# Optimization experiments

Hardware: AMD Instinct MI355X
Metric: run time of the kernel (lower is better)

Reference implementation:

```python
import jax, jax.numpy as jnp
import numpy as np

QMIN, QMAX = -128.0, 127.0  # int8 range


def _fake_int_cast(t):
    # Emulates .to(torch.int8) on an already-clamped float tensor:
    # truncation toward zero, then back to float.
    return jnp.trunc(t)


def setup_inputs() -> dict:
    key = jax.random.key(0)
    k_x, k_w, k_ws, k_is, k_b = jax.random.split(key, 5)
    B, S, IN, OUT = 4, 2048, 4096, 4096
    x = jax.random.normal(k_x, (B, S, IN), dtype=jnp.float32)
    # quant_weight buffer holds int8 values (stored here as fp32 integers),
    # produced by quantizing a dense fp weight with per-out-channel scales.
    weight_scale = jax.random.uniform(k_ws, (OUT, 1), dtype=jnp.float32, minval=0.005, maxval=0.02)
    w_fp = jax.random.normal(k_w, (OUT, IN), dtype=jnp.float32) * 0.02
    quant_weight = jnp.trunc(jnp.clip(w_fp / weight_scale, QMIN, QMAX))
    input_scale = jax.random.uniform(k_is, (1,), dtype=jnp.float32, minval=0.01, maxval=0.03)
    bias = jax.random.normal(k_b, (OUT,), dtype=jnp.float32)
    return {"x": x, "quant_weight": quant_weight, "weight_scale": weight_scale,
            "input_scale": input_scale, "bias": bias}


def reference(x, quant_weight, weight_scale, input_scale, bias):
    # quantize input: clamp(x/scale) -> int8 (trunc toward zero) -> float
    quant_input = _fake_int_cast(jnp.clip(x / input_scale, QMIN, QMAX))
    # int8 matmul performed in fp32: [B,S,IN] @ [OUT,IN]^T -> [B,S,OUT]
    quant_output = jnp.einsum("bsi,oi->bso", quant_input, quant_weight)
    # dequantize with combined per-out-channel scale, viewed [1,1,OUT]
    scale = (weight_scale * input_scale).reshape((1,) * (quant_output.ndim - 1) + (-1,))
    output = quant_output * scale
    output = output + bias
    return output
```

## Files before the change

### kernel.cpp

```cpp
#include <hip/hip_runtime.h>


using v4i = __attribute__((ext_vector_type(4))) int;

typedef const __attribute__((address_space(1))) signed char gc_t;
typedef __attribute__((address_space(3))) signed char lc_t;

constexpr int BM = 256;
constexpr int BN = 256;
constexpr int BK = 128;
constexpr int TILE_BYTES = BM * BK;


__device__ __forceinline__ int quant4(const float4 f, float s) {
    int a = (int)fminf(fmaxf(f.x / s, -128.0f), 127.0f);
    int b = (int)fminf(fmaxf(f.y / s, -128.0f), 127.0f);
    int c = (int)fminf(fmaxf(f.z / s, -128.0f), 127.0f);
    int d = (int)fminf(fmaxf(f.w / s, -128.0f), 127.0f);
    return (a & 0xff) | ((b & 0xff) << 8) | ((c & 0xff) << 16) | ((d & 0xff) << 24);
}

__global__ void quant_x_kernel(const float4* __restrict__ x,
                               const float* __restrict__ scale,
                               int* __restrict__ out, int n4) {
    const float s = scale[0];
    int i = blockIdx.x * blockDim.x + threadIdx.x;
    if (i >= n4) return;
    out[i] = quant4(x[i], s);
}

__global__ void quant_w_kernel(const float4* __restrict__ w,
                               int* __restrict__ out, int n4) {
    int i = blockIdx.x * blockDim.x + threadIdx.x;
    if (i >= n4) return;
    float4 f = w[i];
    out[i] = ((int)f.x & 0xff) | (((int)f.y & 0xff) << 8) |
             (((int)f.z & 0xff) << 16) | (((int)f.w & 0xff) << 24);
}


#define STAGE_TILE(dstbuf, kbyte)                                              \
    do {                                                                       \
        const signed char* _pa = pA + (size_t)(kbyte);                         \
        const signed char* _pb = pB + (size_t)(kbyte);                         \
        lc_t* _la = (lc_t*)(smem + (dstbuf) * (2 * TILE_BYTES) +               \
                            (wid * 8) * BK);                                   \
        lc_t* _lb = (lc_t*)(smem + (dstbuf) * (2 * TILE_BYTES) + TILE_BYTES +  \
                            (wid * 8) * BK);                                   \
        _Pragma("unroll")                                                      \
        for (int c = 0; c < 4; ++c) {                                          \
            __builtin_amdgcn_global_load_lds(                                  \
                (gc_t*)(_pa + (size_t)(c * 64) * Kz), _la + c * 64 * BK,       \
                16, 0, 0);                                                     \
            __builtin_amdgcn_global_load_lds(                                  \
                (gc_t*)(_pb + (size_t)(c * 64) * Kz), _lb + c * 64 * BK,       \
                16, 0, 0);                                                     \
        }                                                                      \
    } while (0)

__global__ __launch_bounds__(512, 2) void gemm_i8_kernel(
    const signed char* __restrict__ Aq,
    const signed char* __restrict__ Wq,
    const float* __restrict__ wscale,
    const float* __restrict__ iscale,
    const float* __restrict__ bias,
    float* __restrict__ C,
    int M, int N, int K)
{
    __shared__ signed char smem[2 * 2 * TILE_BYTES];

    const int tid  = threadIdx.x;
    const int wid  = tid >> 6;
    const int lane = tid & 63;
    const int wm   = (wid >> 2) * 128;
    const int wn   = (wid & 3) * 64;

    const int nwg = gridDim.x;
    int wg = blockIdx.x;
    if ((nwg & 7) == 0) wg = (wg & 7) * (nwg >> 3) + (wg >> 3);
    const int ntx = N / BN;
    const int m0 = (wg / ntx) * BM;
    const int n0 = (wg % ntx) * BN;

    const int srow   = lane >> 3;
    const int gchunk = (lane & 7) ^ srow;

    const int fr = lane & 15;
    const int qh = lane >> 4;
    const int coff0 = ((0 * 4 + qh) ^ (fr & 7)) * 16;
    const int coff1 = ((1 * 4 + qh) ^ (fr & 7)) * 16;

    v4i acc[8][4];
#pragma unroll
    for (int i = 0; i < 8; ++i)
#pragma unroll
        for (int j = 0; j < 4; ++j) acc[i][j] = (v4i){0, 0, 0, 0};

    const size_t Kz = (size_t)K;
    const signed char* pA = Aq + (size_t)(m0 + wid * 8 + srow) * Kz + gchunk * 16;
    const signed char* pB = Wq + (size_t)(n0 + wid * 8 + srow) * Kz + gchunk * 16;

    const int NT = K / BK;

    STAGE_TILE(0, 0);
    STAGE_TILE(1, BK);

    for (int t = 0; t < NT; ++t) {
        const int cur = t & 1;
        if (t + 1 < NT) {
            asm volatile("s_waitcnt vmcnt(8)" ::: "memory");
        } else {
            asm volatile("s_waitcnt vmcnt(0)" ::: "memory");
        }
        __builtin_amdgcn_s_barrier();

        const signed char* Ab = smem + cur * (2 * TILE_BYTES);
        const signed char* Bb = Ab + TILE_BYTES;

        v4i bf[4][2];
        v4i af[2][2];

#pragma unroll
        for (int p = 0; p < 4; ++p) {
            if (p == 0) {
#pragma unroll
                for (int nt = 0; nt < 4; ++nt) {
                    const signed char* br = Bb + (size_t)(wn + nt * 16 + fr) * BK;
                    bf[nt][0] = *(const v4i*)(br + coff0);
                    bf[nt][1] = *(const v4i*)(br + coff1);
                }
            }
#pragma unroll
            for (int i = 0; i < 2; ++i) {
                const signed char* ar =
                    Ab + (size_t)(wm + (2 * p + i) * 16 + fr) * BK;
                af[i][0] = *(const v4i*)(ar + coff0);
                af[i][1] = *(const v4i*)(ar + coff1);
            }
            __builtin_amdgcn_s_barrier();
            __builtin_amdgcn_sched_barrier(0);
            __builtin_amdgcn_s_setprio(1);
#pragma unroll
            for (int s = 0; s < 2; ++s)
#pragma unroll
                for (int i = 0; i < 2; ++i)
#pragma unroll
                    for (int nt = 0; nt < 4; ++nt)
                        acc[2 * p + i][nt] = __builtin_amdgcn_mfma_i32_16x16x64_i8(
                            af[i][s], bf[nt][s], acc[2 * p + i][nt], 0, 0, 0);
            __builtin_amdgcn_s_setprio(0);
            __builtin_amdgcn_sched_barrier(0);
            __builtin_amdgcn_s_barrier();
        }

        if (t + 2 < NT) {
            asm volatile("" ::: "memory");
            STAGE_TILE(cur, (size_t)(t + 2) * BK);
            asm volatile("" ::: "memory");
        }
    }

    const float is = iscale[0];
#pragma unroll
    for (int nt = 0; nt < 4; ++nt) {
        const int col = n0 + wn + nt * 16 + fr;
        const float sc = wscale[col] * is;
        const float bv = bias[col];
#pragma unroll
        for (int mt = 0; mt < 8; ++mt) {
            const size_t rbase = (size_t)(m0 + wm + mt * 16 + qh * 4);
#pragma unroll
            for (int r = 0; r < 4; ++r) {
                C[(rbase + r) * N + col] = (float)acc[mt][nt][r] * sc + bv;
            }
        }
    }
}


extern "C" void kernel_launch(void* const* d_in, const int* in_sizes, int n_in,
                              void* d_out, int out_size, void* d_ws, size_t ws_size,
                              hipStream_t stream) {
    const float* x  = (const float*)d_in[0];
    const float* qw = (const float*)d_in[1];
    const float* ws = (const float*)d_in[2];
    const float* is = (const float*)d_in[3];
    const float* bs = (const float*)d_in[4];
    float* out = (float*)d_out;

    const int nx = in_sizes[0];
    const int nw = in_sizes[1];
    const int N  = in_sizes[4];
    const int K  = nw / N;
    const int M  = nx / K;

    signed char* xq = (signed char*)d_ws;
    signed char* wq = (signed char*)d_ws + (size_t)nx;

    quant_x_kernel<<<nx / 4 / 256, 256, 0, stream>>>(
        (const float4*)x, is, (int*)xq, nx / 4);
    quant_w_kernel<<<nw / 4 / 256, 256, 0, stream>>>(
        (const float4*)qw, (int*)wq, nw / 4);

    dim3 grid((M / BM) * (N / BN));
    gemm_i8_kernel<<<grid, 512, 0, stream>>>(xq, wq, ws, is, bs, out, M, N, K);
}
```

Before: 411.7 us.

## Interleave global-to-LDS prefetch chunks across MFMA phases of the int8 GEMM

Splits the tile staging into per-chunk A and B loads and issues them between the four compute phases of each K-step, instead of one bulk staging after all compute. B for tile j+2 is written into the current buffer as soon as its fragments are in registers. A chunks are written once the phases that read them are finished. This spreads memory traffic across the loop to overlap with MFMA work, and the vmcnt wait is adjusted to match. The cost is a more fragile buffer-reuse ordering and a slightly different barrier layout, dropping the trailing barrier of the last phase.

```diff
diff --git a/kernel.cpp b/kernel.cpp
--- a/kernel.cpp
+++ b/kernel.cpp
@@ -39,24 +39,44 @@
 }
 
 
-#define STAGE_TILE(dstbuf, kbyte)                                              \
-    do {                                                                       \
-        const signed char* _pa = pA + (size_t)(kbyte);                         \
-        const signed char* _pb = pB + (size_t)(kbyte);                         \
-        lc_t* _la = (lc_t*)(smem + (dstbuf) * (2 * TILE_BYTES) +               \
-                            (wid * 8) * BK);                                   \
-        lc_t* _lb = (lc_t*)(smem + (dstbuf) * (2 * TILE_BYTES) + TILE_BYTES +  \
-                            (wid * 8) * BK);                                   \
-        _Pragma("unroll")                                                      \
-        for (int c = 0; c < 4; ++c) {                                          \
-            __builtin_amdgcn_global_load_lds(                                  \
-                (gc_t*)(_pa + (size_t)(c * 64) * Kz), _la + c * 64 * BK,       \
-                16, 0, 0);                                                     \
-            __builtin_amdgcn_global_load_lds(                                  \
-                (gc_t*)(_pb + (size_t)(c * 64) * Kz), _lb + c * 64 * BK,       \
-                16, 0, 0);                                                     \
-        }                                                                      \
-    } while (0)
+#define SA(buf_, tile_, cc_)                                                   \
+    __builtin_amdgcn_global_load_lds(                                          \
+        (gc_t*)(pA + (size_t)(tile_) * BK + (size_t)((cc_) * 64) * Kz),        \
+        (lc_t*)(smem + (buf_) * (2 * TILE_BYTES) + (wid * 8 + (cc_) * 64) * BK),\
+        16, 0, 0)
+
+#define SB(buf_, tile_, cc_)                                                   \
+    __builtin_amdgcn_global_load_lds(                                          \
+        (gc_t*)(pB + (size_t)(tile_) * BK + (size_t)((cc_) * 64) * Kz),        \
+        (lc_t*)(smem + (buf_) * (2 * TILE_BYTES) + TILE_BYTES +                \
+                (wid * 8 + (cc_) * 64) * BK),                                  \
+        16, 0, 0)
+
+#define PHASE_READS(p_)                                                        \
+    a00 = *(const v4i*)(Ab + (size_t)(wm + (2 * (p_)) * 16 + fr) * BK + coff0);\
+    a01 = *(const v4i*)(Ab + (size_t)(wm + (2 * (p_)) * 16 + fr) * BK + coff1);\
+    a10 = *(const v4i*)(Ab + (size_t)(wm + (2 * (p_) + 1) * 16 + fr) * BK + coff0);\
+    a11 = *(const v4i*)(Ab + (size_t)(wm + (2 * (p_) + 1) * 16 + fr) * BK + coff1);
+
+#define PHASE_MFMA(p_)                                                         \
+    __builtin_amdgcn_s_setprio(1);                                             \
+    _Pragma("unroll")                                                          \
+    for (int nt = 0; nt < 4; ++nt)                                             \
+        acc[2 * (p_)][nt] = __builtin_amdgcn_mfma_i32_16x16x64_i8(             \
+            a00, bf[nt][0], acc[2 * (p_)][nt], 0, 0, 0);                       \
+    _Pragma("unroll")                                                          \
+    for (int nt = 0; nt < 4; ++nt)                                             \
+        acc[2 * (p_) + 1][nt] = __builtin_amdgcn_mfma_i32_16x16x64_i8(         \
+            a10, bf[nt][0], acc[2 * (p_) + 1][nt], 0, 0, 0);                   \
+    _Pragma("unroll")                                                          \
+    for (int nt = 0; nt < 4; ++nt)                                             \
+        acc[2 * (p_)][nt] = __builtin_amdgcn_mfma_i32_16x16x64_i8(             \
+            a01, bf[nt][1], acc[2 * (p_)][nt], 0, 0, 0);                       \
+    _Pragma("unroll")                                                          \
+    for (int nt = 0; nt < 4; ++nt)                                             \
+        acc[2 * (p_) + 1][nt] = __builtin_amdgcn_mfma_i32_16x16x64_i8(         \
+            a11, bf[nt][1], acc[2 * (p_) + 1][nt], 0, 0, 0);                   \
+    __builtin_amdgcn_s_setprio(0);
 
 __global__ __launch_bounds__(512, 2) void gemm_i8_kernel(
     const signed char* __restrict__ Aq,
@@ -102,62 +122,55 @@
 
     const int NT = K / BK;
 
-    STAGE_TILE(0, 0);
-    STAGE_TILE(1, BK);
-
-    for (int t = 0; t < NT; ++t) {
-        const int cur = t & 1;
-        if (t + 1 < NT) {
-            asm volatile("s_waitcnt vmcnt(8)" ::: "memory");
+    SA(0, 0, 0); SA(0, 0, 1); SA(0, 0, 2); SA(0, 0, 3);
+    SB(0, 0, 0); SB(0, 0, 1); SB(0, 0, 2); SB(0, 0, 3);
+    SB(1, 1, 0); SB(1, 1, 1); SB(1, 1, 2); SB(1, 1, 3);
+    SA(1, 1, 0); SA(1, 1, 2);
+
+    for (int j = 0; j < NT; ++j) {
+        const int cur = j & 1;
+        const int nxt = cur ^ 1;
+        const signed char* Ab = smem + cur * (2 * TILE_BYTES);
+        const signed char* Bb = Ab + TILE_BYTES;
+
+        if (j + 1 < NT) {
+            asm volatile("s_waitcnt vmcnt(6)" ::: "memory");
         } else {
             asm volatile("s_waitcnt vmcnt(0)" ::: "memory");
         }
         __builtin_amdgcn_s_barrier();
 
-        const signed char* Ab = smem + cur * (2 * TILE_BYTES);
-        const signed char* Bb = Ab + TILE_BYTES;
-
         v4i bf[4][2];
-        v4i af[2][2];
-
-#pragma unroll
-        for (int p = 0; p < 4; ++p) {
-            if (p == 0) {
-#pragma unroll
-                for (int nt = 0; nt < 4; ++nt) {
-                    const signed char* br = Bb + (size_t)(wn + nt * 16 + fr) * BK;
-                    bf[nt][0] = *(const v4i*)(br + coff0);
-                    bf[nt][1] = *(const v4i*)(br + coff1);
-                }
-            }
-#pragma unroll
-            for (int i = 0; i < 2; ++i) {
-                const signed char* ar =
-                    Ab + (size_t)(wm + (2 * p + i) * 16 + fr) * BK;
-                af[i][0] = *(const v4i*)(ar + coff0);
-                af[i][1] = *(const v4i*)(ar + coff1);
-            }
-            __builtin_amdgcn_s_barrier();
-            __builtin_amdgcn_sched_barrier(0);
-            __builtin_amdgcn_s_setprio(1);
-#pragma unroll
-            for (int s = 0; s < 2; ++s)
-#pragma unroll
-                for (int i = 0; i < 2; ++i)
-#pragma unroll
-                    for (int nt = 0; nt < 4; ++nt)
-                        acc[2 * p + i][nt] = __builtin_amdgcn_mfma_i32_16x16x64_i8(
-                            af[i][s], bf[nt][s], acc[2 * p + i][nt], 0, 0, 0);
-            __builtin_amdgcn_s_setprio(0);
-            __builtin_amdgcn_sched_barrier(0);
-            __builtin_amdgcn_s_barrier();
+        v4i a00, a01, a10, a11;
+
+#pragma unroll
+        for (int nt = 0; nt < 4; ++nt) {
+            const signed char* br = Bb + (size_t)(wn + nt * 16 + fr) * BK;
+            bf[nt][0] = *(const v4i*)(br + coff0);
+            bf[nt][1] = *(const v4i*)(br + coff1);
         }
-
-        if (t + 2 < NT) {
-            asm volatile("" ::: "memory");
-            STAGE_TILE(cur, (size_t)(t + 2) * BK);
-            asm volatile("" ::: "memory");
-        }
+        PHASE_READS(0);
+        if (j + 1 < NT) { SA(nxt, j + 1, 1); SA(nxt, j + 1, 3); }
+        __builtin_amdgcn_s_barrier();
+        PHASE_MFMA(0);
+        __builtin_amdgcn_s_barrier();
+
+        PHASE_READS(1);
+        if (j + 2 < NT) { SB(cur, j + 2, 0); SB(cur, j + 2, 1); }
+        __builtin_amdgcn_s_barrier();
+        PHASE_MFMA(1);
+        __builtin_amdgcn_s_barrier();
+
+        PHASE_READS(2);
+        if (j + 2 < NT) { SB(cur, j + 2, 2); SB(cur, j + 2, 3); }
+        __builtin_amdgcn_s_barrier();
+        PHASE_MFMA(2);
+        __builtin_amdgcn_s_barrier();
+
+        PHASE_READS(3);
+        if (j + 2 < NT) { SA(cur, j + 2, 0); SA(cur, j + 2, 2); }
+        __builtin_amdgcn_s_barrier();
+        PHASE_MFMA(3);
     }
 
     const float is = iscale[0];
```

Measured after the change: 389.0 us. 1.06x faster.
